# Optimization experiments

Measured on AMD Instinct MI355X. Metric: run time of the kernel, lower is better.

Reference implementation:

```python
import jax, jax.numpy as jnp
import numpy as np

N_DIRS = 32  # number of projection directions


def gram_schmidt(x):
    # x: [B, n, D]; sequential Gram-Schmidt; normalized basis vectors are
    # detached (stop_gradient) as in the torch original.
    B, n, D = x.shape
    xs = jnp.swapaxes(x, 0, 1)  # [n, B, D]
    basis0 = jnp.zeros((n, B, D), dtype=x.dtype)

    def step(carry, w):
        basis, i = carry

        def proj(j, wv):
            b = basis[j]  # rows >= i are zero and contribute nothing
            return wv - b * jnp.sum(wv * b, axis=-1, keepdims=True)

        w_o = jax.lax.fori_loop(0, n, proj, w)
        w_sg = jax.lax.stop_gradient(w_o)
        w_hat = w_sg / jnp.linalg.norm(w_sg, axis=-1, keepdims=True)
        basis = jax.lax.dynamic_update_slice(basis, w_hat[None], (i, 0, 0))
        return (basis, i + 1), w_o

    (_, _), x_orth = jax.lax.scan(step, (basis0, jnp.int32(0)), xs)
    return jnp.swapaxes(x_orth, 0, 1)  # [B, n, D]


def setup_inputs() -> dict:
    key = jax.random.key(0)
    k = jax.random.split(key, 6)
    B = 2048
    IN_LP = 32 * 26       # 832 = linear_projection_x_dim * 26
    IMG = 28 * 28         # 784
    IN_NET = 2 * IMG      # 1568
    OUT_NET = N_DIRS * IMG  # 25088

    x_distorted = jax.random.normal(k[0], (B, IN_LP), dtype=jnp.float32)
    x_restored = jax.random.uniform(k[1], (B, 1, 28, 28), dtype=jnp.float32)

    s1 = 1.0 / np.sqrt(IN_LP)
    W_lp = jax.random.uniform(k[2], (IMG, IN_LP), jnp.float32, -s1, s1)
    b_lp = jax.random.uniform(k[3], (IMG,), jnp.float32, -s1, s1)

    s2 = 1.0 / np.sqrt(IN_NET)
    W_net = jax.random.uniform(k[4], (OUT_NET, IN_NET), jnp.float32, -s2, s2)
    b_net = jax.random.uniform(k[5], (OUT_NET,), jnp.float32, -s2, s2)

    return {"x_distorted": x_distorted, "x_restored": x_restored,
            "W_lp": W_lp, "b_lp": b_lp, "W_net": W_net, "b_net": b_net}


def reference(x_distorted, x_restored, W_lp, b_lp, W_net, b_net):
    B = x_distorted.shape[0]
    xd = x_distorted.reshape(B, -1) @ W_lp.T + b_lp      # [B, 784]
    xd = xd.reshape(B, 1, 28, 28)
    x = jnp.concatenate([xd, x_restored], axis=1)        # [B, 2, 28, 28]
    x = (x - 0.5) / 0.2
    w_mat = (x.reshape(B, -1) @ W_net.T + b_net) * 0.2   # [B, n_dirs*784]
    w_mat = w_mat.reshape(B, N_DIRS, -1)                 # [B, n_dirs, 784]
    return gram_schmidt(w_mat)
```

## Files before the change

kernel.cpp:

```cpp
#include <hip/hip_runtime.h>
#include <hip/hip_bf16.h>
#include <stdint.h>


typedef short s16x8 __attribute__((ext_vector_type(8)));
typedef float f32x4 __attribute__((ext_vector_type(4)));

#define GL_LDS16(gptr, lptr)                                                   \
    __builtin_amdgcn_global_load_lds(                                          \
        (const __attribute__((address_space(1))) void*)(gptr),                 \
        (__attribute__((address_space(3))) void*)(lptr), 16, 0, 0)

__global__ __launch_bounds__(512, 2) void gemm_mfma_256(
    const __hip_bfloat16* __restrict__ A, const __hip_bfloat16* __restrict__ B,
    const float* __restrict__ bias, float* __restrict__ C,
    int M, int N, int K)
{
    __shared__ __align__(16) short lds[3][16384];

    const int t = threadIdx.x;
    const int l = t & 63;
    const int wv = t >> 6;
    const int wm = wv >> 2;
    const int wn = wv & 3;

    const int f  = blockIdx.x;
    const int xb = f >> 3;
    const int yb = f & 7;
    const int m0 = yb * 256;
    const int n0 = xb * 256;

    const short* As = (const short*)A;
    const short* Bs = (const short*)B;

    const int colE = ((((l & 3) << 4) ^ (l & 48)) >> 1);
    const size_t baseA0 = (size_t)(m0 + wv * 32 +  0 + (l >> 2)) * K + colE;
    const size_t baseA1 = (size_t)(m0 + wv * 32 + 16 + (l >> 2)) * K + colE;
    const size_t baseB0 = (size_t)(n0 + wv * 32 +  0 + (l >> 2)) * K + colE;
    const size_t baseB1 = (size_t)(n0 + wv * 32 + 16 + (l >> 2)) * K + colE;
    const int dst0 = (wv * 2 + 0) * 512;
    const int dst1 = (wv * 2 + 1) * 512;

    const int xk   = ((l >> 4) * 16) ^ ((l & 12) << 2);
    const int aoff = ((wm * 128 + (l & 15)) * 64 + xk) >> 1;
    const int boff = ((wn * 64  + (l & 15)) * 64 + xk) >> 1;

    f32x4 acc[8][4] = {};

#define STAGE_TILE(buf, T)                                                     \
    do {                                                                       \
        short* bA_ = &lds[buf][0];                                             \
        short* bB_ = &lds[buf][8192];                                          \
        const size_t ko_ = (size_t)(T) * 32;                                   \
        GL_LDS16(As + baseA0 + ko_, bA_ + dst0);                               \
        GL_LDS16(As + baseA1 + ko_, bA_ + dst1);                               \
        GL_LDS16(Bs + baseB0 + ko_, bB_ + dst0);                               \
        GL_LDS16(Bs + baseB1 + ko_, bB_ + dst1);                               \
    } while (0)

    const int NT = K >> 5;
    STAGE_TILE(0, 0);
    STAGE_TILE(1, 1);

    int cur = 0;
    for (int kt = 0; kt < NT; ++kt) {
        if (kt < NT - 1) asm volatile("s_waitcnt vmcnt(4)");
        else             asm volatile("s_waitcnt vmcnt(0)");
        __builtin_amdgcn_sched_barrier(0);
        asm volatile("" ::: "memory");
        __builtin_amdgcn_s_barrier();
        asm volatile("" ::: "memory");
        __builtin_amdgcn_sched_barrier(0);

        if (kt + 2 < NT) {
            int nb = cur + 2; if (nb >= 3) nb -= 3;
            STAGE_TILE(nb, kt + 2);
        }

        const short* bA = &lds[cur][0];
        const short* bB = &lds[cur][8192];
        s16x8 af[8], bf[4];
        #pragma unroll
        for (int mi = 0; mi < 8; ++mi)
            af[mi] = *(const s16x8*)&bA[aoff + mi * 512];
        #pragma unroll
        for (int ni = 0; ni < 4; ++ni)
            bf[ni] = *(const s16x8*)&bB[boff + ni * 512];

        __builtin_amdgcn_s_setprio(1);
        #pragma unroll
        for (int mi = 0; mi < 8; ++mi)
            #pragma unroll
            for (int ni = 0; ni < 4; ++ni)
                acc[mi][ni] = __builtin_amdgcn_mfma_f32_16x16x32_bf16(
                    af[mi], bf[ni], acc[mi][ni], 0, 0, 0);
        __builtin_amdgcn_s_setprio(0);

        ++cur; if (cur >= 3) cur = 0;
    }
#undef STAGE_TILE

    const int row0 = m0 + wm * 128 + ((l >> 4) << 2);
    const int col0 = n0 + wn * 64 + (l & 15);
    #pragma unroll
    for (int ni = 0; ni < 4; ++ni) {
        const int n = col0 + ni * 16;
        const float bn = bias[n];
        #pragma unroll
        for (int mi = 0; mi < 8; ++mi) {
            const int r0 = row0 + mi * 16;
            #pragma unroll
            for (int r = 0; r < 4; ++r)
                C[(size_t)(r0 + r) * N + n] = (acc[mi][ni][r] + bn) * 0.2f;
        }
    }
}

__global__ __launch_bounds__(256) void f32_to_bf16(
    const float* __restrict__ in, __hip_bfloat16* __restrict__ out, int n4)
{
    int i = blockIdx.x * blockDim.x + threadIdx.x;
    const int stride = gridDim.x * blockDim.x;
    for (; i < n4; i += stride) {
        float4 v = ((const float4*)in)[i];
        __hip_bfloat16 o[4] = {
            __float2bfloat16(v.x), __float2bfloat16(v.y),
            __float2bfloat16(v.z), __float2bfloat16(v.w)};
        *(ushort4*)&out[(size_t)i * 4] = *(const ushort4*)o;
    }
}

#define TILE_M 64
#define TILE_N 64
#define TILE_K 16
#define LDS_STRIDE 72

__global__ __launch_bounds__(256) void gemm_nt_lp(
    const float* __restrict__ A, const float* __restrict__ B,
    const float* __restrict__ bias, __hip_bfloat16* __restrict__ C,
    int M, int N, int K, int ldc)
{
    __shared__ float As[TILE_K][LDS_STRIDE];
    __shared__ float Bsh[TILE_K][LDS_STRIDE];

    const int t  = threadIdx.x;
    const int tx = t & 15;
    const int ty = t >> 4;
    const int m0 = blockIdx.y * TILE_M;
    const int n0 = blockIdx.x * TILE_N;
    const int lrow = t >> 2;
    const int lk   = (t & 3) << 2;

    float acc[4][4] = {};

    for (int kt = 0; kt < K; kt += TILE_K) {
        float4 av = *(const float4*)(A + (size_t)(m0 + lrow) * K + kt + lk);
        float4 bv = make_float4(0.f, 0.f, 0.f, 0.f);
        if (n0 + lrow < N)
            bv = *(const float4*)(B + (size_t)(n0 + lrow) * K + kt + lk);

        __syncthreads();
        As[lk + 0][lrow] = av.x; As[lk + 1][lrow] = av.y;
        As[lk + 2][lrow] = av.z; As[lk + 3][lrow] = av.w;
        Bsh[lk + 0][lrow] = bv.x; Bsh[lk + 1][lrow] = bv.y;
        Bsh[lk + 2][lrow] = bv.z; Bsh[lk + 3][lrow] = bv.w;
        __syncthreads();

        #pragma unroll
        for (int k = 0; k < TILE_K; ++k) {
            float4 a = *(const float4*)&As[k][ty << 2];
            float4 b = *(const float4*)&Bsh[k][tx << 2];
            acc[0][0] += a.x * b.x; acc[0][1] += a.x * b.y;
            acc[0][2] += a.x * b.z; acc[0][3] += a.x * b.w;
            acc[1][0] += a.y * b.x; acc[1][1] += a.y * b.y;
            acc[1][2] += a.y * b.z; acc[1][3] += a.y * b.w;
            acc[2][0] += a.z * b.x; acc[2][1] += a.z * b.y;
            acc[2][2] += a.z * b.z; acc[2][3] += a.z * b.w;
            acc[3][0] += a.w * b.x; acc[3][1] += a.w * b.y;
            acc[3][2] += a.w * b.z; acc[3][3] += a.w * b.w;
        }
    }

    #pragma unroll
    for (int j = 0; j < 4; ++j) {
        int n = n0 + (tx << 2) + j;
        if (n < N) {
            float bn = bias[n];
            #pragma unroll
            for (int i = 0; i < 4; ++i) {
                float v = (acc[i][j] + bn - 0.5f) / 0.2f;
                C[(size_t)(m0 + (ty << 2) + i) * ldc + n] = __float2bfloat16(v);
            }
        }
    }
}

__global__ __launch_bounds__(256) void build_restored(
    const float* __restrict__ xr, __hip_bfloat16* __restrict__ x)
{
    const int b = blockIdx.x;
    const int t = threadIdx.x;
    if (t < 196) {
        float4 v = *(const float4*)(xr + (size_t)b * 784 + (t << 2));
        __hip_bfloat16 o[4] = {
            __float2bfloat16((v.x - 0.5f) / 0.2f),
            __float2bfloat16((v.y - 0.5f) / 0.2f),
            __float2bfloat16((v.z - 0.5f) / 0.2f),
            __float2bfloat16((v.w - 0.5f) / 0.2f)};
        *(ushort4*)&x[(size_t)b * 1568 + 784 + (t << 2)] = *(const ushort4*)o;
    }
}

#define GS_N 32
#define GS_D 784

__global__ __launch_bounds__(256, 4) void gram_solve(
    const float* __restrict__ out, float* __restrict__ Mws)
{
    __shared__ __align__(16) short Wc[GS_N * 64];
    __shared__ float Gs[GS_N][GS_N + 1];
    __shared__ float Ms[GS_N][GS_N + 1];
    __shared__ float Ld[GS_N];

    const int t = threadIdx.x;
    const int l = t & 63;
    const int w = t >> 6;
    const float* row0 = out + (size_t)blockIdx.x * (GS_N * GS_D);

    const int wr = w >> 1, wc2 = w & 1;
    const int ra = wr * 16 + (l & 15);
    const int rb = wc2 * 16 + (l & 15);
    const int kg = l >> 4;

    f32x4 acc = {};

    for (int k0 = 0; k0 < 832; k0 += 64) {
        #pragma unroll
        for (int hh = 0; hh < 2; ++hh) {
            const int h   = t + hh * 256;
            const int r   = h >> 4;
            const int hg  = h & 15;
            const int col = k0 + (hg << 2);
            ushort4 u = make_ushort4(0, 0, 0, 0);
            if (col < GS_D) {
                float4 v = *(const float4*)(row0 + r * GS_D + col);
                __hip_bfloat16 hb[4] = {
                    __float2bfloat16(v.x), __float2bfloat16(v.y),
                    __float2bfloat16(v.z), __float2bfloat16(v.w)};
                u = *(const ushort4*)hb;
            }
            const int gp = (hg >> 1) ^ (r & 7);
            *(ushort4*)&Wc[(r << 6) + (gp << 3) + ((hg & 1) << 2)] = u;
        }
        __syncthreads();

        #pragma unroll
        for (int s = 0; s < 2; ++s) {
            const int ga = ((s << 2) + kg) ^ (ra & 7);
            const int gb = ((s << 2) + kg) ^ (rb & 7);
            s16x8 af = *(const s16x8*)&Wc[(ra << 6) + (ga << 3)];
            s16x8 bf = *(const s16x8*)&Wc[(rb << 6) + (gb << 3)];
            acc = __builtin_amdgcn_mfma_f32_16x16x32_bf16(af, bf, acc, 0, 0, 0);
        }
        __syncthreads();
    }

    {
        const int di = wr * 16 + (l >> 4) * 4;
        const int dj = wc2 * 16 + (l & 15);
        #pragma unroll
        for (int r = 0; r < 4; ++r) Gs[di + r][dj] = acc[r];
    }
    for (int z = t; z < GS_N * (GS_N + 1); z += 256) ((float*)Ms)[z] = 0.f;
    __syncthreads();

    for (int k = 0; k < GS_N; ++k) {
        const float sk = sqrtf(Gs[k][k]);
        if (t == k) Ld[k] = sk;
        if (t > k && t < GS_N) Gs[t][k] /= sk;
        __syncthreads();
        if (t > k && t < GS_N) {
            const float lik = Gs[t][k];
            for (int j = k + 1; j <= t; ++j)
                Gs[t][j] -= lik * Gs[j][k];
        }
        __syncthreads();
    }

    if (t < GS_N) {
        const int j = t;
        Ms[j][j] = 1.0f / Ld[j];
        for (int i = j + 1; i < GS_N; ++i) {
            float a = 0.f;
            for (int k = j; k < i; ++k)
                a += Gs[i][k] * Ms[k][j];
            Ms[i][j] = -a / Ld[i];
        }
        for (int i = j + 1; i < GS_N; ++i)
            Ms[i][j] *= Ld[i];
    }
    __syncthreads();

    {
        const int i = t >> 3, j0 = (t & 7) << 2;
        float4 mv = make_float4(Ms[i][j0], Ms[i][j0 + 1],
                                Ms[i][j0 + 2], Ms[i][j0 + 3]);
        *(float4*)(Mws + (size_t)blockIdx.x * 1024 + (t << 2)) = mv;
    }
}

__global__ __launch_bounds__(256, 8) void gs_apply(
    float* __restrict__ out, const float* __restrict__ Mws)
{
    __shared__ float4 Wf[GS_N][28];
    __shared__ float  Ml[GS_N][36];

    const int t = threadIdx.x;
    const int b = blockIdx.y;
    const int k0 = blockIdx.x * 112;
    float* row0 = out + (size_t)b * (GS_N * GS_D);

    {
        float4 mv = *(const float4*)(Mws + (size_t)b * 1024 + (t << 2));
        const int i = t >> 3, j0 = (t & 7) << 2;
        *(float4*)&Ml[i][j0] = mv;
    }
    #pragma unroll
    for (int hh = 0; hh < 4; ++hh) {
        const int h = t + hh * 256;
        const int r = h >> 5, c = h & 31;
        if (c < 28)
            Wf[r][c] = *(const float4*)(row0 + r * GS_D + k0 + (c << 2));
    }
    __syncthreads();

    const int rg = t >> 5;
    const int c4 = t & 31;
    if (c4 < 28) {
        const int i0 = rg << 2;
        float4 c0 = Wf[i0 + 0][c4];
        float4 c1 = Wf[i0 + 1][c4];
        float4 c2 = Wf[i0 + 2][c4];
        float4 c3 = Wf[i0 + 3][c4];
        for (int j = 0; j < GS_N - 1; ++j) {
            if (j > i0 + 2) break;
            const float4 wj = Wf[j][c4];
            const float m0 = (i0 + 0 > j) ? Ml[i0 + 0][j] : 0.f;
            const float m1 = (i0 + 1 > j) ? Ml[i0 + 1][j] : 0.f;
            const float m2 = (i0 + 2 > j) ? Ml[i0 + 2][j] : 0.f;
            const float m3 = (i0 + 3 > j) ? Ml[i0 + 3][j] : 0.f;
            c0.x += m0 * wj.x; c0.y += m0 * wj.y;
            c0.z += m0 * wj.z; c0.w += m0 * wj.w;
            c1.x += m1 * wj.x; c1.y += m1 * wj.y;
            c1.z += m1 * wj.z; c1.w += m1 * wj.w;
            c2.x += m2 * wj.x; c2.y += m2 * wj.y;
            c2.z += m2 * wj.z; c2.w += m2 * wj.w;
            c3.x += m3 * wj.x; c3.y += m3 * wj.y;
            c3.z += m3 * wj.z; c3.w += m3 * wj.w;
        }
        *(float4*)(row0 + (i0 + 0) * GS_D + k0 + (c4 << 2)) = c0;
        *(float4*)(row0 + (i0 + 1) * GS_D + k0 + (c4 << 2)) = c1;
        *(float4*)(row0 + (i0 + 2) * GS_D + k0 + (c4 << 2)) = c2;
        *(float4*)(row0 + (i0 + 3) * GS_D + k0 + (c4 << 2)) = c3;
    }
}

extern "C" void kernel_launch(void* const* d_in, const int* in_sizes, int n_in,
                              void* d_out, int out_size, void* d_ws, size_t ws_size,
                              hipStream_t stream)
{
    const float* xd   = (const float*)d_in[0];
    const float* xr   = (const float*)d_in[1];
    const float* Wlp  = (const float*)d_in[2];
    const float* blp  = (const float*)d_in[3];
    const float* Wnet = (const float*)d_in[4];
    const float* bnet = (const float*)d_in[5];
    float* out = (float*)d_out;

    const int B = 2048, IN_LP = 832, IMG = 784, IN_NET = 1568, OUT = 32 * 784;

    __hip_bfloat16* Wnet_bf = (__hip_bfloat16*)d_ws;
    __hip_bfloat16* x_bf =
        (__hip_bfloat16*)((char*)d_ws + (size_t)OUT * IN_NET * 2);
    float* Mws = (float*)d_ws;

    f32_to_bf16<<<2048, 256, 0, stream>>>(Wnet, Wnet_bf, OUT * IN_NET / 4);

    gemm_nt_lp<<<dim3((IMG + TILE_N - 1) / TILE_N, B / TILE_M), 256, 0, stream>>>(
        xd, Wlp, blp, x_bf, B, IMG, IN_LP, IN_NET);

    build_restored<<<B, 256, 0, stream>>>(xr, x_bf);

    gemm_mfma_256<<<dim3(784), 512, 0, stream>>>(
        x_bf, Wnet_bf, bnet, out, B, OUT, IN_NET);

    gram_solve<<<B, 256, 0, stream>>>(out, Mws);

    gs_apply<<<dim3(7, B), 256, 0, stream>>>(out, Mws);
}
```

Baseline: 477.8 us.

## Split GEMM k-step into two phases interleaving LDS reads, staging, and MFMA

Each k-iteration of the MFMA GEMM is split into two halves. Each half loads part of the A fragments from LDS, issues either the A or the B global-to-LDS staging for tile kt+2, and then runs 16 MFMAs, with extra workgroup barriers between phases. The LDS XOR swizzle pattern is also changed, and launch bounds drop from 2 to 1 blocks per CU. The aim is to spread memory traffic across the loop and overlap it with MFMA work while reducing LDS bank conflicts. The cost is two to three extra barriers per iteration and possibly lower occupancy.

Result: faster. 466.4 us (-2.4%).

```diff
diff --git a/kernel.cpp b/kernel.cpp
--- a/kernel.cpp
+++ b/kernel.cpp
@@ -11,7 +11,15 @@
         (const __attribute__((address_space(1))) void*)(gptr),                 \
         (__attribute__((address_space(3))) void*)(lptr), 16, 0, 0)
 
-__global__ __launch_bounds__(512, 2) void gemm_mfma_256(
+#define PHASE_BARRIER()                                                        \
+    do {                                                                       \
+        asm volatile("" ::: "memory");                                         \
+        __builtin_amdgcn_s_barrier();                                          \
+        asm volatile("" ::: "memory");                                         \
+        __builtin_amdgcn_sched_barrier(0);                                     \
+    } while (0)
+
+__global__ __launch_bounds__(512, 1) void gemm_mfma_256(
     const __hip_bfloat16* __restrict__ A, const __hip_bfloat16* __restrict__ B,
     const float* __restrict__ bias, float* __restrict__ C,
     int M, int N, int K)
@@ -33,7 +41,7 @@
     const short* As = (const short*)A;
     const short* Bs = (const short*)B;
 
-    const int colE = ((((l & 3) << 4) ^ (l & 48)) >> 1);
+    const int colE = ((((l & 3) << 4) ^ ((l & 24) << 1)) >> 1);
     const size_t baseA0 = (size_t)(m0 + wv * 32 +  0 + (l >> 2)) * K + colE;
     const size_t baseA1 = (size_t)(m0 + wv * 32 + 16 + (l >> 2)) * K + colE;
     const size_t baseB0 = (size_t)(n0 + wv * 32 +  0 + (l >> 2)) * K + colE;
@@ -41,64 +49,82 @@
     const int dst0 = (wv * 2 + 0) * 512;
     const int dst1 = (wv * 2 + 1) * 512;
 
-    const int xk   = ((l >> 4) * 16) ^ ((l & 12) << 2);
+    const int xk   = ((l >> 4) * 16) ^ ((l & 6) << 3);
     const int aoff = ((wm * 128 + (l & 15)) * 64 + xk) >> 1;
     const int boff = ((wn * 64  + (l & 15)) * 64 + xk) >> 1;
 
     f32x4 acc[8][4] = {};
 
-#define STAGE_TILE(buf, T)                                                     \
+#define STAGE_A(buf, T)                                                        \
     do {                                                                       \
         short* bA_ = &lds[buf][0];                                             \
-        short* bB_ = &lds[buf][8192];                                          \
         const size_t ko_ = (size_t)(T) * 32;                                   \
         GL_LDS16(As + baseA0 + ko_, bA_ + dst0);                               \
         GL_LDS16(As + baseA1 + ko_, bA_ + dst1);                               \
+    } while (0)
+#define STAGE_B(buf, T)                                                        \
+    do {                                                                       \
+        short* bB_ = &lds[buf][8192];                                          \
+        const size_t ko_ = (size_t)(T) * 32;                                   \
         GL_LDS16(Bs + baseB0 + ko_, bB_ + dst0);                               \
         GL_LDS16(Bs + baseB1 + ko_, bB_ + dst1);                               \
     } while (0)
 
     const int NT = K >> 5;
-    STAGE_TILE(0, 0);
-    STAGE_TILE(1, 1);
+    STAGE_A(0, 0); STAGE_B(0, 0);
+    STAGE_A(1, 1); STAGE_B(1, 1);
 
     int cur = 0;
     for (int kt = 0; kt < NT; ++kt) {
         if (kt < NT - 1) asm volatile("s_waitcnt vmcnt(4)");
         else             asm volatile("s_waitcnt vmcnt(0)");
         __builtin_amdgcn_sched_barrier(0);
-        asm volatile("" ::: "memory");
-        __builtin_amdgcn_s_barrier();
-        asm volatile("" ::: "memory");
-        __builtin_amdgcn_sched_barrier(0);
-
-        if (kt + 2 < NT) {
-            int nb = cur + 2; if (nb >= 3) nb -= 3;
-            STAGE_TILE(nb, kt + 2);
-        }
-
+        PHASE_BARRIER();
+
+        int nb = cur + 2; if (nb >= 3) nb -= 3;
         const short* bA = &lds[cur][0];
         const short* bB = &lds[cur][8192];
-        s16x8 af[8], bf[4];
-        #pragma unroll
-        for (int mi = 0; mi < 8; ++mi)
-            af[mi] = *(const s16x8*)&bA[aoff + mi * 512];
+
+        s16x8 bf[4], af[4];
         #pragma unroll
         for (int ni = 0; ni < 4; ++ni)
             bf[ni] = *(const s16x8*)&bB[boff + ni * 512];
-
+        #pragma unroll
+        for (int mi = 0; mi < 4; ++mi)
+            af[mi] = *(const s16x8*)&bA[aoff + mi * 512];
+        if (kt + 2 < NT) STAGE_A(nb, kt + 2);
+
+        PHASE_BARRIER();
         __builtin_amdgcn_s_setprio(1);
         #pragma unroll
-        for (int mi = 0; mi < 8; ++mi)
+        for (int mi = 0; mi < 4; ++mi)
             #pragma unroll
             for (int ni = 0; ni < 4; ++ni)
                 acc[mi][ni] = __builtin_amdgcn_mfma_f32_16x16x32_bf16(
                     af[mi], bf[ni], acc[mi][ni], 0, 0, 0);
         __builtin_amdgcn_s_setprio(0);
+        PHASE_BARRIER();
+
+        s16x8 ag[4];
+        #pragma unroll
+        for (int mi = 0; mi < 4; ++mi)
+            ag[mi] = *(const s16x8*)&bA[aoff + (mi + 4) * 512];
+        if (kt + 2 < NT) STAGE_B(nb, kt + 2);
+
+        PHASE_BARRIER();
+        __builtin_amdgcn_s_setprio(1);
+        #pragma unroll
+        for (int mi = 0; mi < 4; ++mi)
+            #pragma unroll
+            for (int ni = 0; ni < 4; ++ni)
+                acc[mi + 4][ni] = __builtin_amdgcn_mfma_f32_16x16x32_bf16(
+                    ag[mi], bf[ni], acc[mi + 4][ni], 0, 0, 0);
+        __builtin_amdgcn_s_setprio(0);
 
         ++cur; if (cur >= 3) cur = 0;
     }
-#undef STAGE_TILE
+#undef STAGE_A
+#undef STAGE_B
 
     const int row0 = m0 + wm * 128 + ((l >> 4) << 2);
     const int col0 = n0 + wn * 64 + (l & 15);
```
